# Kernel optimization log

Hardware: AMD Instinct MI355X
Metric: run time of the kernel (lower is better)

Reference implementation:

```python
import jax, jax.numpy as jnp
import numpy as np

N, D, E = 50000, 128, 800000


def setup_inputs() -> dict:
    key = jax.random.key(0)
    ks = jax.random.split(key, 12)
    x0 = jax.random.normal(ks[0], (N, D), dtype=jnp.float32)
    x1 = jax.random.normal(ks[1], (N, D), dtype=jnp.float32)
    edge_index = jax.random.randint(ks[2], (2, E), 0, N, dtype=jnp.int64)
    s = 0.05
    W1 = jax.random.normal(ks[3], (D, D), dtype=jnp.float32) * s
    b1 = jax.random.normal(ks[4], (D,), dtype=jnp.float32) * s
    W2 = jax.random.normal(ks[5], (D, D), dtype=jnp.float32) * s
    b2 = jax.random.normal(ks[6], (D,), dtype=jnp.float32) * s
    a1_w = jax.random.normal(ks[7], (D,), dtype=jnp.float32) * s
    a1_b = jax.random.normal(ks[8], (), dtype=jnp.float32) * s
    a2_w = jax.random.normal(ks[9], (D,), dtype=jnp.float32) * s
    a2_b = jax.random.normal(ks[10], (), dtype=jnp.float32) * s
    return {"x0": x0, "x1": x1, "edge_index": edge_index,
            "W1": W1, "b1": b1, "W2": W2, "b2": b2,
            "a1_w": a1_w, "a1_b": a1_b, "a2_w": a2_w, "a2_b": a2_b}


def reference(x0, x1, edge_index, W1, b1, W2, b2, a1_w, a1_b, a2_w, a2_b):
    # LeakyReLU(0.2) applied to both projections
    lrelu = lambda v: jnp.where(v >= 0, v, 0.2 * v)
    x0_i = lrelu(x0 @ W1.T + b1)          # [N, D]
    x0_j = lrelu(x0 @ W2.T + b2)          # [N, D]
    a1 = x0_i @ a1_w + a1_b               # [N]
    a2 = x0_j @ a2_w + a2_b               # [N]
    src, dst = edge_index[0], edge_index[1]
    # sigmoid(a_1 + a_2.T) evaluated only at the sparse edge indices
    att = jax.nn.sigmoid(a1[src] + a2[dst])            # [E]
    msg = att[:, None] * x0_j[dst]                     # [E, D]
    out = jax.ops.segment_sum(msg, src, num_segments=x0.shape[0])  # sparse.mm
    return out + x0
```

## Files before the change

kernel.cpp:

```cpp
#include <hip/hip_runtime.h>
#include <hip/hip_bf16.h>

typedef unsigned int u32;
typedef unsigned short u16;

#define DIM 128
#define LWS 136
#define CHUNK 2048

typedef __bf16 bfrag __attribute__((ext_vector_type(8)));
typedef float  facc  __attribute__((ext_vector_type(4)));

__device__ __forceinline__ float2 bfpair(u32 u) {
    union { u32 i; float f; } lo, hi;
    lo.i = (u & 0xFFFFu) << 16;
    hi.i = u & 0xFFFF0000u;
    return make_float2(lo.f, hi.f);
}
__device__ __forceinline__ float bf1(u16 h) {
    union { u32 i; float f; } a; a.i = ((u32)h) << 16; return a.f;
}
__device__ __forceinline__ u16 f2bf(float f) {
    __hip_bfloat16 h = __float2bfloat16(f);
    return *reinterpret_cast<u16*>(&h);
}
__device__ __forceinline__ u32 packbf(float x, float y) {
    return (u32)f2bf(x) | ((u32)f2bf(y) << 16);
}

template<bool BF16>
__device__ __forceinline__ float ldf(const void* p, int i) {
    if constexpr (BF16) return bf1(((const u16*)p)[i]);
    else                return ((const float*)p)[i];
}

template<bool BF16>
__device__ __forceinline__ bfrag ldfrag(const void* base, int row, int elt) {
    if constexpr (BF16) {
        const uint4* p = (const uint4*)((const u16*)base + (size_t)row * DIM + elt);
        return __builtin_bit_cast(bfrag, *p);
    } else {
        const float4* p = (const float4*)((const float*)base + (size_t)row * DIM + elt);
        float4 f0 = p[0], f1 = p[1];
        uint4 u = make_uint4(packbf(f0.x, f0.y), packbf(f0.z, f0.w),
                             packbf(f1.x, f1.y), packbf(f1.z, f1.w));
        return __builtin_bit_cast(bfrag, u);
    }
}

__global__ __launch_bounds__(64) void sniff_kernel(const u32* __restrict__ x0w,
                                                   const int* __restrict__ eiw,
                                                   int* __restrict__ flags) {
    int l = threadIdx.x;
    u32 w = x0w[l];
    u32 ef = (w >> 7) & 0xFF;
    bool inr = (ef >= 99 && ef <= 141);
    unsigned long long m1 = __ballot(inr);
    bool zodd = (eiw[2 * l + 1] == 0);
    unsigned long long m2 = __ballot(zodd);
    if (l == 0) {
        flags[0] = (__popcll(m1) >= 48) ? 1 : 0;
        flags[1] = (__popcll(m2) >= 32) ? 1 : 0;
    }
}

template<bool BF16>
__global__ __launch_bounds__(256) void proj_kernel(
    const void* __restrict__ x0v,
    const void* __restrict__ W1v, const void* __restrict__ b1v,
    const void* __restrict__ W2v, const void* __restrict__ b2v,
    const void* __restrict__ a1wv, const void* __restrict__ a1bv,
    const void* __restrict__ a2wv, const void* __restrict__ a2bv,
    u16* __restrict__ xj, float* __restrict__ a1, float* __restrict__ a2,
    const int* __restrict__ flags, int n, int nchunk, int bpg)
{
    if ((flags[0] != 0) != BF16) return;
    __shared__ u16 lw[128 * LWS];

    const int t   = threadIdx.x;
    const int grp = blockIdx.x / bpg;
    const int cb  = blockIdx.x % bpg;

    const void* Wv  = grp ? W2v  : W1v;
    const void* bv  = grp ? b2v  : b1v;
    const void* awv = grp ? a2wv : a1wv;
    const void* abv = grp ? a2bv : a1bv;
    float* aout     = grp ? a2   : a1;

    for (int j = t; j < 2048; j += 256) {
        int r = j >> 4, c = j & 15;
        uint4 u;
        if constexpr (BF16) {
            u = *(const uint4*)((const u16*)Wv + (size_t)r * DIM + c * 8);
        } else {
            const float4* p = (const float4*)((const float*)Wv + (size_t)r * DIM + c * 8);
            float4 f0 = p[0], f1 = p[1];
            u = make_uint4(packbf(f0.x, f0.y), packbf(f0.z, f0.w),
                           packbf(f1.x, f1.y), packbf(f1.z, f1.w));
        }
        *(uint4*)(lw + (size_t)r * LWS + c * 8) = u;
    }
    __syncthreads();

    const int wid = t >> 6, l = t & 63;
    const int chunk = cb * 4 + wid;
    if (chunk >= nchunk) return;
    const int r0 = chunk * 32;
    const int lr = l & 15;
    const int q  = l >> 4;

    bfrag a[2][4];
    #pragma unroll
    for (int rt = 0; rt < 2; ++rt) {
        int row = min(r0 + rt * 16 + lr, n - 1);
        #pragma unroll
        for (int k = 0; k < 4; ++k)
            a[rt][k] = ldfrag<BF16>(x0v, row, k * 32 + q * 8);
    }

    facc acc[2][8];
    #pragma unroll
    for (int rt = 0; rt < 2; ++rt)
        #pragma unroll
        for (int ct = 0; ct < 8; ++ct)
            acc[rt][ct] = (facc){0.f, 0.f, 0.f, 0.f};

    #pragma unroll
    for (int ct = 0; ct < 8; ++ct) {
        bfrag bb[4];
        const u16* lrow = lw + (size_t)(ct * 16 + lr) * LWS;
        #pragma unroll
        for (int k = 0; k < 4; ++k)
            bb[k] = *(const bfrag*)(lrow + k * 32 + q * 8);
        #pragma unroll
        for (int rt = 0; rt < 2; ++rt)
            #pragma unroll
            for (int k = 0; k < 4; ++k)
                acc[rt][ct] = __builtin_amdgcn_mfma_f32_16x16x32_bf16(
                    a[rt][k], bb[k], acc[rt][ct], 0, 0, 0);
    }

    float s[2][4] = {{0.f,0.f,0.f,0.f},{0.f,0.f,0.f,0.f}};
    #pragma unroll
    for (int ct = 0; ct < 8; ++ct) {
        float bc  = ldf<BF16>(bv,  ct * 16 + lr);
        float awc = ldf<BF16>(awv, ct * 16 + lr);
        #pragma unroll
        for (int rt = 0; rt < 2; ++rt)
            #pragma unroll
            for (int reg = 0; reg < 4; ++reg) {
                float v = acc[rt][ct][reg] + bc;
                v = v >= 0.f ? v : 0.2f * v;
                int row = r0 + rt * 16 + q * 4 + reg;
                if (grp && row < n)
                    xj[(size_t)row * DIM + ct * 16 + lr] = f2bf(v);
                s[rt][reg] = fmaf(v, awc, s[rt][reg]);
            }
    }
    #pragma unroll
    for (int off = 1; off < 16; off <<= 1)
        #pragma unroll
        for (int rt = 0; rt < 2; ++rt)
            #pragma unroll
            for (int reg = 0; reg < 4; ++reg)
                s[rt][reg] += __shfl_xor(s[rt][reg], off);
    if (lr == 0) {
        float ab = ldf<BF16>(abv, 0);
        #pragma unroll
        for (int rt = 0; rt < 2; ++rt)
            #pragma unroll
            for (int reg = 0; reg < 4; ++reg) {
                int row = r0 + rt * 16 + q * 4 + reg;
                if (row < n) aout[row] = s[rt][reg] + ab;
            }
    }
}


__global__ __launch_bounds__(256) void countA_kernel(
    const int* __restrict__ ei, u32* __restrict__ keys0,
    int* __restrict__ cnt, const int* __restrict__ flags, int ne, int nblk)
{
    __shared__ int h[256];
    const int b = blockIdx.x, t = threadIdx.x;
    h[t] = 0;
    __syncthreads();
    const bool i64 = flags[1] != 0;
    const int base = b * CHUNK;
    #pragma unroll
    for (int r = 0; r < CHUNK / 256; ++r) {
        int i = base + r * 256 + t;
        if (i < ne) {
            int src = i64 ? ei[2 * i] : ei[i];
            int dst = i64 ? ei[2 * (ne + i)] : ei[ne + i];
            u32 key = ((u32)src << 16) | (u32)dst;
            keys0[i] = key;
            atomicAdd(&h[(key >> 16) & 0xFF], 1);
        }
    }
    __syncthreads();
    cnt[t * nblk + b] = h[t];
}

__global__ __launch_bounds__(256) void countB_kernel(
    const u32* __restrict__ kin, int* __restrict__ cnt, int ne, int nblk)
{
    __shared__ int h[256];
    const int b = blockIdx.x, t = threadIdx.x;
    h[t] = 0;
    __syncthreads();
    const int base = b * CHUNK;
    #pragma unroll
    for (int r = 0; r < CHUNK / 256; ++r) {
        int i = base + r * 256 + t;
        if (i < ne) atomicAdd(&h[kin[i] >> 24], 1);
    }
    __syncthreads();
    cnt[t * nblk + b] = h[t];
}

__global__ __launch_bounds__(256) void scan1_kernel(
    const int* __restrict__ cnt, int* __restrict__ off,
    int* __restrict__ tot, int nblk)
{
    __shared__ int v[512];
    const int d = blockIdx.x, t = threadIdx.x;
    int c0 = (t < nblk) ? cnt[d * nblk + t] : 0;
    int c1 = (t + 256 < nblk) ? cnt[d * nblk + t + 256] : 0;
    v[t] = c0; v[t + 256] = c1;
    __syncthreads();
    for (int s = 1; s < 512; s <<= 1) {
        int a0 = v[t],      b0 = (t >= s) ? v[t - s] : 0;
        int a1 = v[t + 256], b1 = (t + 256 >= s) ? v[t + 256 - s] : 0;
        __syncthreads();
        v[t] = a0 + b0; v[t + 256] = a1 + b1;
        __syncthreads();
    }
    if (t < nblk)       off[d * nblk + t]       = v[t] - c0;
    if (t + 256 < nblk) off[d * nblk + t + 256] = v[t + 256] - c1;
    if (t == 0) tot[d] = v[511];
}

__global__ __launch_bounds__(256) void scan2_kernel(
    const int* __restrict__ tot, int* __restrict__ basev)
{
    __shared__ int v[256];
    const int t = threadIdx.x;
    int c = tot[t];
    v[t] = c;
    __syncthreads();
    for (int s = 1; s < 256; s <<= 1) {
        int a = v[t], b = (t >= s) ? v[t - s] : 0;
        __syncthreads();
        v[t] = a + b;
        __syncthreads();
    }
    basev[t] = v[t] - c;
}

__global__ __launch_bounds__(256) void reorderA_kernel(
    const u32* __restrict__ kin, u32* __restrict__ kout,
    const int* __restrict__ off, const int* __restrict__ basev,
    int ne, int nblk)
{
    __shared__ u32 kk[CHUNK];
    __shared__ int boff[256];
    __shared__ int bcnt[256];
    const int b = blockIdx.x, t = threadIdx.x;
    const int base = b * CHUNK;
    const int cntk = min(CHUNK, ne - base);
    #pragma unroll
    for (int r = 0; r < CHUNK / 256; ++r) {
        int i = r * 256 + t;
        if (i < cntk) kk[i] = kin[base + i];
    }
    boff[t] = basev[t] + off[t * nblk + b];
    bcnt[t] = 0;
    __syncthreads();
    #pragma unroll
    for (int r = 0; r < CHUNK / 256; ++r) {
        int i = r * 256 + t;
        if (i < cntk) {
            u32 key = kk[i];
            int d = (key >> 16) & 0xFF;
            int rk = atomicAdd(&bcnt[d], 1);
            kout[boff[d] + rk] = key;
        }
    }
}

__global__ __launch_bounds__(64) void reorderB_kernel(
    const u32* __restrict__ kin, u32* __restrict__ kout,
    const int* __restrict__ off, const int* __restrict__ basev,
    int ne, int nblk)
{
    __shared__ u16 M[256 * 65];
    __shared__ u32 kk[CHUNK];
    __shared__ int boff[256];
    const int b = blockIdx.x, t = threadIdx.x;
    u32* M32 = (u32*)M;
    for (int j = t; j < 256 * 65 / 2; j += 64) M32[j] = 0;
    const int base = b * CHUNK;
    const int cntk = min(CHUNK, ne - base);
    for (int r = 0; r < CHUNK / 64; ++r) {
        int i = r * 64 + t;
        if (i < cntk) kk[i] = kin[base + i];
    }
    for (int d = t; d < 256; d += 64) boff[d] = basev[d] + off[d * nblk + b];
    __syncthreads();
    const int k0 = t * (CHUNK / 64);
    for (int j = 0; j < CHUNK / 64; ++j) {
        int i = k0 + j;
        if (i < cntk) { int d = kk[i] >> 24; M[d * 65 + t] += 1; }
    }
    __syncthreads();
    for (int rr = 0; rr < 4; ++rr) {
        int d = t + rr * 64;
        int run = 0, rb = d * 65;
        for (int j = 0; j < 64; ++j) {
            int c = M[rb + j]; M[rb + j] = (u16)run; run += c;
        }
    }
    __syncthreads();
    for (int j = 0; j < CHUNK / 64; ++j) {
        int i = k0 + j;
        if (i < cntk) {
            u32 key = kk[i];
            int d = key >> 24;
            int rk = M[d * 65 + t];
            M[d * 65 + t] = (u16)(rk + 1);
            kout[boff[d] + rk] = key;
        }
    }
}

__global__ __launch_bounds__(256) void ptr_kernel(
    const u32* __restrict__ skeys, int* __restrict__ ptr, int ne, int n)
{
    int i = blockIdx.x * 256 + threadIdx.x;
    if (i >= ne) return;
    int s = (int)(skeys[i] >> 16);
    if (i == 0) {
        for (int j = 0; j <= s; ++j) ptr[j] = 0;
    } else {
        int sp = (int)(skeys[i - 1] >> 16);
        for (int j = sp + 1; j <= s; ++j) ptr[j] = i;
    }
    if (i == ne - 1) {
        for (int j = s + 1; j <= n; ++j) ptr[j] = ne;
    }
}

template<bool BF16>
__global__ __launch_bounds__(256) void gather_kernel(
    const int* __restrict__ ptr, const u32* __restrict__ skeys,
    const float* __restrict__ a1, const float* __restrict__ a2,
    const u32* __restrict__ xjw, const void* __restrict__ x0v,
    void* __restrict__ outv, const int* __restrict__ flags, int n)
{
    if ((flags[0] != 0) != BF16) return;
    int s = blockIdx.x * 4 + (threadIdx.x >> 6);
    int l = threadIdx.x & 63;
    if (s >= n) return;

    float2 acc0, acc1;
    if constexpr (BF16) acc0 = bfpair(((const u32*)x0v)[(size_t)s * 64 + l]);
    else                acc0 = ((const float2*)x0v)[(size_t)s * 64 + l];
    acc1 = make_float2(0.f, 0.f);
    const float a1s = a1[s];

    int k = ptr[s], end = ptr[s + 1];

    while (k + 8 <= end) {
        u32 r[8];
        #pragma unroll
        for (int j = 0; j < 8; ++j) r[j] = skeys[k + j];
        u32 w[8]; float av[8];
        #pragma unroll
        for (int j = 0; j < 8; ++j) w[j] = xjw[(size_t)(r[j] & 0xFFFFu) * 64 + l];
        #pragma unroll
        for (int j = 0; j < 8; ++j) av[j] = a2[r[j] & 0xFFFFu];
        #pragma unroll
        for (int j = 0; j < 8; ++j) {
            float att = 1.0f / (1.0f + __expf(-(a1s + av[j])));
            float2 xv = bfpair(w[j]);
            if (j & 1) { acc1.x = fmaf(att, xv.x, acc1.x);
                         acc1.y = fmaf(att, xv.y, acc1.y); }
            else       { acc0.x = fmaf(att, xv.x, acc0.x);
                         acc0.y = fmaf(att, xv.y, acc0.y); }
        }
        k += 8;
    }
    if (k + 4 <= end) {
        u32 r[4];
        #pragma unroll
        for (int j = 0; j < 4; ++j) r[j] = skeys[k + j];
        u32 w[4]; float av[4];
        #pragma unroll
        for (int j = 0; j < 4; ++j) w[j] = xjw[(size_t)(r[j] & 0xFFFFu) * 64 + l];
        #pragma unroll
        for (int j = 0; j < 4; ++j) av[j] = a2[r[j] & 0xFFFFu];
        #pragma unroll
        for (int j = 0; j < 4; ++j) {
            float att = 1.0f / (1.0f + __expf(-(a1s + av[j])));
            float2 xv = bfpair(w[j]);
            if (j & 1) { acc1.x = fmaf(att, xv.x, acc1.x);
                         acc1.y = fmaf(att, xv.y, acc1.y); }
            else       { acc0.x = fmaf(att, xv.x, acc0.x);
                         acc0.y = fmaf(att, xv.y, acc0.y); }
        }
        k += 4;
    }
    for (; k < end; ++k) {
        u32 cur = skeys[k];
        float att = 1.0f / (1.0f + __expf(-(a1s + a2[cur & 0xFFFFu])));
        float2 xv = bfpair(xjw[(size_t)(cur & 0xFFFFu) * 64 + l]);
        acc0.x = fmaf(att, xv.x, acc0.x);
        acc0.y = fmaf(att, xv.y, acc0.y);
    }
    acc0.x += acc1.x;
    acc0.y += acc1.y;

    if constexpr (BF16) ((u32*)outv)[(size_t)s * 64 + l] = packbf(acc0.x, acc0.y);
    else                ((float2*)outv)[(size_t)s * 64 + l] = acc0;
}

extern "C" void kernel_launch(void* const* d_in, const int* in_sizes, int n_in,
                              void* d_out, int out_size, void* d_ws, size_t ws_size,
                              hipStream_t stream)
{
    const void* x0  = d_in[0];
    const int*  ei  = (const int*)d_in[2];
    const void* W1  = d_in[3];
    const void* b1  = d_in[4];
    const void* W2  = d_in[5];
    const void* b2  = d_in[6];
    const void* a1w = d_in[7];
    const void* a1b = d_in[8];
    const void* a2w = d_in[9];
    const void* a2b = d_in[10];

    const int n = in_sizes[0] / DIM;
    const int e = in_sizes[2] / 2;
    const int nblk = (e + CHUNK - 1) / CHUNK;

    char* ws = (char*)d_ws;
    int* flags = (int*)ws;
    size_t off = 1024;
    u16* xj = (u16*)(ws + off);
    off += (size_t)n * DIM * sizeof(u16);   off = (off + 255) & ~(size_t)255;
    float* a1 = (float*)(ws + off);
    off += (size_t)n * sizeof(float);       off = (off + 255) & ~(size_t)255;
    float* a2 = (float*)(ws + off);
    off += (size_t)n * sizeof(float);       off = (off + 255) & ~(size_t)255;
    u32* keys0 = (u32*)(ws + off);
    off += (size_t)e * sizeof(u32);         off = (off + 255) & ~(size_t)255;
    u32* keys1 = (u32*)(ws + off);
    off += (size_t)e * sizeof(u32);         off = (off + 255) & ~(size_t)255;
    u32* keys2 = (u32*)(ws + off);
    off += (size_t)e * sizeof(u32);         off = (off + 255) & ~(size_t)255;
    int* cntA = (int*)(ws + off);
    off += (size_t)256 * nblk * sizeof(int); off = (off + 255) & ~(size_t)255;
    int* offA = (int*)(ws + off);
    off += (size_t)256 * nblk * sizeof(int); off = (off + 255) & ~(size_t)255;
    int* cntB = (int*)(ws + off);
    off += (size_t)256 * nblk * sizeof(int); off = (off + 255) & ~(size_t)255;
    int* offB = (int*)(ws + off);
    off += (size_t)256 * nblk * sizeof(int); off = (off + 255) & ~(size_t)255;
    int* totA = (int*)(ws + off);  off += 1024;
    int* baseA = (int*)(ws + off); off += 1024;
    int* totB = (int*)(ws + off);  off += 1024;
    int* baseB = (int*)(ws + off); off += 1024;
    int* ptr = (int*)(ws + off);
    off += (size_t)(n + 1) * sizeof(int);

    sniff_kernel<<<1, 64, 0, stream>>>((const u32*)x0, ei, flags);

    const int nchunk = (n + 31) / 32;
    const int bpg = (nchunk + 3) / 4;
    proj_kernel<true ><<<2 * bpg, 256, 0, stream>>>(x0, W1, b1, W2, b2, a1w, a1b,
                                                    a2w, a2b, xj, a1, a2, flags, n, nchunk, bpg);
    proj_kernel<false><<<2 * bpg, 256, 0, stream>>>(x0, W1, b1, W2, b2, a1w, a1b,
                                                    a2w, a2b, xj, a1, a2, flags, n, nchunk, bpg);

    countA_kernel<<<nblk, 256, 0, stream>>>(ei, keys0, cntA, flags, e, nblk);
    scan1_kernel<<<256, 256, 0, stream>>>(cntA, offA, totA, nblk);
    scan2_kernel<<<1, 256, 0, stream>>>(totA, baseA);
    reorderA_kernel<<<nblk, 256, 0, stream>>>(keys0, keys1, offA, baseA, e, nblk);
    countB_kernel<<<nblk, 256, 0, stream>>>(keys1, cntB, e, nblk);
    scan1_kernel<<<256, 256, 0, stream>>>(cntB, offB, totB, nblk);
    scan2_kernel<<<1, 256, 0, stream>>>(totB, baseB);
    reorderB_kernel<<<nblk, 64, 0, stream>>>(keys1, keys2, offB, baseB, e, nblk);
    ptr_kernel<<<(e + 255) / 256, 256, 0, stream>>>(keys2, ptr, e, n);

    int gblocks = (n + 3) / 4;
    gather_kernel<true ><<<gblocks, 256, 0, stream>>>(ptr, keys2, a1, a2,
                                                      (const u32*)xj, x0, d_out, flags, n);
    gather_kernel<false><<<gblocks, 256, 0, stream>>>(ptr, keys2, a1, a2,
                                                      (const u32*)xj, x0, d_out, flags, n);
}
```

Baseline: 230.5 us.

## Replace two-pass radix sort with one bucket pass plus per-bucket local sort

The two-pass LSD radix sort by source node (count/scan/reorder twice plus a ptr kernel) becomes a single global pass on the high byte. It is followed by one block per high-byte bucket that locally sorts by the low byte and writes the CSR row pointers directly. That bucket kernel also computes the sigmoid attention per edge and stores (dst, att) pairs, so the gather no longer reads a1/a2 or evaluates the exp. This removes several launches and a full pass over the keys, but writes 8-byte records instead of 4-byte keys, and each bucket (~3k edges) is handled by a single 256-thread block.

```diff
diff --git a/kernel.cpp b/kernel.cpp
--- a/kernel.cpp
+++ b/kernel.cpp
@@ -177,7 +177,7 @@
 }
 
 
-__global__ __launch_bounds__(256) void countA_kernel(
+__global__ __launch_bounds__(256) void countH_kernel(
     const int* __restrict__ ei, u32* __restrict__ keys0,
     int* __restrict__ cnt, const int* __restrict__ flags, int ne, int nblk)
 {
@@ -195,25 +195,8 @@
             int dst = i64 ? ei[2 * (ne + i)] : ei[ne + i];
             u32 key = ((u32)src << 16) | (u32)dst;
             keys0[i] = key;
-            atomicAdd(&h[(key >> 16) & 0xFF], 1);
+            atomicAdd(&h[key >> 24], 1);
         }
-    }
-    __syncthreads();
-    cnt[t * nblk + b] = h[t];
-}
-
-__global__ __launch_bounds__(256) void countB_kernel(
-    const u32* __restrict__ kin, int* __restrict__ cnt, int ne, int nblk)
-{
-    __shared__ int h[256];
-    const int b = blockIdx.x, t = threadIdx.x;
-    h[t] = 0;
-    __syncthreads();
-    const int base = b * CHUNK;
-    #pragma unroll
-    for (int r = 0; r < CHUNK / 256; ++r) {
-        int i = base + r * 256 + t;
-        if (i < ne) atomicAdd(&h[kin[i] >> 24], 1);
     }
     __syncthreads();
     cnt[t * nblk + b] = h[t];
@@ -258,103 +241,77 @@
     basev[t] = v[t] - c;
 }
 
-__global__ __launch_bounds__(256) void reorderA_kernel(
+__global__ __launch_bounds__(256) void reorderH_kernel(
     const u32* __restrict__ kin, u32* __restrict__ kout,
     const int* __restrict__ off, const int* __restrict__ basev,
     int ne, int nblk)
 {
-    __shared__ u32 kk[CHUNK];
     __shared__ int boff[256];
     __shared__ int bcnt[256];
     const int b = blockIdx.x, t = threadIdx.x;
     const int base = b * CHUNK;
-    const int cntk = min(CHUNK, ne - base);
-    #pragma unroll
-    for (int r = 0; r < CHUNK / 256; ++r) {
-        int i = r * 256 + t;
-        if (i < cntk) kk[i] = kin[base + i];
-    }
     boff[t] = basev[t] + off[t * nblk + b];
     bcnt[t] = 0;
     __syncthreads();
     #pragma unroll
     for (int r = 0; r < CHUNK / 256; ++r) {
-        int i = r * 256 + t;
-        if (i < cntk) {
-            u32 key = kk[i];
-            int d = (key >> 16) & 0xFF;
+        int i = base + r * 256 + t;
+        if (i < ne) {
+            u32 key = kin[i];
+            int d = key >> 24;
             int rk = atomicAdd(&bcnt[d], 1);
             kout[boff[d] + rk] = key;
         }
     }
 }
 
-__global__ __launch_bounds__(64) void reorderB_kernel(
-    const u32* __restrict__ kin, u32* __restrict__ kout,
-    const int* __restrict__ off, const int* __restrict__ basev,
-    int ne, int nblk)
-{
-    __shared__ u16 M[256 * 65];
-    __shared__ u32 kk[CHUNK];
-    __shared__ int boff[256];
+__global__ __launch_bounds__(256) void bucket_kernel(
+    const u32* __restrict__ keys1, const int* __restrict__ basev,
+    const int* __restrict__ tot, const float* __restrict__ a1,
+    const float* __restrict__ a2, int* __restrict__ ptr,
+    uint2* __restrict__ sorted, int n)
+{
+    __shared__ int cnt[256];
+    __shared__ int sc[256];
+    __shared__ int cur[256];
     const int b = blockIdx.x, t = threadIdx.x;
-    u32* M32 = (u32*)M;
-    for (int j = t; j < 256 * 65 / 2; j += 64) M32[j] = 0;
-    const int base = b * CHUNK;
-    const int cntk = min(CHUNK, ne - base);
-    for (int r = 0; r < CHUNK / 64; ++r) {
-        int i = r * 64 + t;
-        if (i < cntk) kk[i] = kin[base + i];
-    }
-    for (int d = t; d < 256; d += 64) boff[d] = basev[d] + off[d * nblk + b];
-    __syncthreads();
-    const int k0 = t * (CHUNK / 64);
-    for (int j = 0; j < CHUNK / 64; ++j) {
-        int i = k0 + j;
-        if (i < cntk) { int d = kk[i] >> 24; M[d * 65 + t] += 1; }
-    }
-    __syncthreads();
-    for (int rr = 0; rr < 4; ++rr) {
-        int d = t + rr * 64;
-        int run = 0, rb = d * 65;
-        for (int j = 0; j < 64; ++j) {
-            int c = M[rb + j]; M[rb + j] = (u16)run; run += c;
-        }
-    }
-    __syncthreads();
-    for (int j = 0; j < CHUNK / 64; ++j) {
-        int i = k0 + j;
-        if (i < cntk) {
-            u32 key = kk[i];
-            int d = key >> 24;
-            int rk = M[d * 65 + t];
-            M[d * 65 + t] = (u16)(rk + 1);
-            kout[boff[d] + rk] = key;
-        }
-    }
-}
-
-__global__ __launch_bounds__(256) void ptr_kernel(
-    const u32* __restrict__ skeys, int* __restrict__ ptr, int ne, int n)
-{
-    int i = blockIdx.x * 256 + threadIdx.x;
-    if (i >= ne) return;
-    int s = (int)(skeys[i] >> 16);
-    if (i == 0) {
-        for (int j = 0; j <= s; ++j) ptr[j] = 0;
-    } else {
-        int sp = (int)(skeys[i - 1] >> 16);
-        for (int j = sp + 1; j <= s; ++j) ptr[j] = i;
-    }
-    if (i == ne - 1) {
-        for (int j = s + 1; j <= n; ++j) ptr[j] = ne;
+    const int base = basev[b];
+    const int size = tot[b];
+    cnt[t] = 0;
+    __syncthreads();
+    for (int i = t; i < size; i += 256)
+        atomicAdd(&cnt[(keys1[base + i] >> 16) & 0xFF], 1);
+    __syncthreads();
+    int c = cnt[t];
+    sc[t] = c;
+    __syncthreads();
+    for (int s = 1; s < 256; s <<= 1) {
+        int a = sc[t], add = (t >= s) ? sc[t - s] : 0;
+        __syncthreads();
+        sc[t] = a + add;
+        __syncthreads();
+    }
+    int ex = sc[t] - c;
+    cur[t] = ex;
+    int sg = (b << 8) + t;
+    if (sg <= n) ptr[sg] = base + ex;
+    __syncthreads();
+    for (int i = t; i < size; i += 256) {
+        u32 key = keys1[base + i];
+        int j   = (key >> 16) & 0xFF;
+        int rk  = atomicAdd(&cur[j], 1);
+        int src = (int)(key >> 16);
+        int dst = (int)(key & 0xFFFFu);
+        float av  = a1[src] + a2[dst];
+        float att = 1.0f / (1.0f + __expf(-av));
+        uint2 rec; rec.x = (u32)dst; rec.y = __float_as_uint(att);
+        sorted[base + rk] = rec;
     }
 }
 
 template<bool BF16>
 __global__ __launch_bounds__(256) void gather_kernel(
-    const int* __restrict__ ptr, const u32* __restrict__ skeys,
-    const float* __restrict__ a1, const float* __restrict__ a2,
+    const int* __restrict__ ptr, const uint2* __restrict__ sorted,
     const u32* __restrict__ xjw, const void* __restrict__ x0v,
     void* __restrict__ outv, const int* __restrict__ flags, int n)
 {
@@ -367,22 +324,19 @@
     if constexpr (BF16) acc0 = bfpair(((const u32*)x0v)[(size_t)s * 64 + l]);
     else                acc0 = ((const float2*)x0v)[(size_t)s * 64 + l];
     acc1 = make_float2(0.f, 0.f);
-    const float a1s = a1[s];
 
     int k = ptr[s], end = ptr[s + 1];
 
     while (k + 8 <= end) {
-        u32 r[8];
-        #pragma unroll
-        for (int j = 0; j < 8; ++j) r[j] = skeys[k + j];
-        u32 w[8]; float av[8];
-        #pragma unroll
-        for (int j = 0; j < 8; ++j) w[j] = xjw[(size_t)(r[j] & 0xFFFFu) * 64 + l];
-        #pragma unroll
-        for (int j = 0; j < 8; ++j) av[j] = a2[r[j] & 0xFFFFu];
+        uint2 r[8];
+        #pragma unroll
+        for (int j = 0; j < 8; ++j) r[j] = sorted[k + j];
+        u32 w[8];
+        #pragma unroll
+        for (int j = 0; j < 8; ++j) w[j] = xjw[(size_t)r[j].x * 64 + l];
         #pragma unroll
         for (int j = 0; j < 8; ++j) {
-            float att = 1.0f / (1.0f + __expf(-(a1s + av[j])));
+            float att = __uint_as_float(r[j].y);
             float2 xv = bfpair(w[j]);
             if (j & 1) { acc1.x = fmaf(att, xv.x, acc1.x);
                          acc1.y = fmaf(att, xv.y, acc1.y); }
@@ -392,17 +346,15 @@
         k += 8;
     }
     if (k + 4 <= end) {
-        u32 r[4];
-        #pragma unroll
-        for (int j = 0; j < 4; ++j) r[j] = skeys[k + j];
-        u32 w[4]; float av[4];
-        #pragma unroll
-        for (int j = 0; j < 4; ++j) w[j] = xjw[(size_t)(r[j] & 0xFFFFu) * 64 + l];
-        #pragma unroll
-        for (int j = 0; j < 4; ++j) av[j] = a2[r[j] & 0xFFFFu];
+        uint2 r[4];
+        #pragma unroll
+        for (int j = 0; j < 4; ++j) r[j] = sorted[k + j];
+        u32 w[4];
+        #pragma unroll
+        for (int j = 0; j < 4; ++j) w[j] = xjw[(size_t)r[j].x * 64 + l];
         #pragma unroll
         for (int j = 0; j < 4; ++j) {
-            float att = 1.0f / (1.0f + __expf(-(a1s + av[j])));
+            float att = __uint_as_float(r[j].y);
             float2 xv = bfpair(w[j]);
             if (j & 1) { acc1.x = fmaf(att, xv.x, acc1.x);
                          acc1.y = fmaf(att, xv.y, acc1.y); }
@@ -412,9 +364,9 @@
         k += 4;
     }
     for (; k < end; ++k) {
-        u32 cur = skeys[k];
-        float att = 1.0f / (1.0f + __expf(-(a1s + a2[cur & 0xFFFFu])));
-        float2 xv = bfpair(xjw[(size_t)(cur & 0xFFFFu) * 64 + l]);
+        uint2 cur = sorted[k];
+        float att = __uint_as_float(cur.y);
+        float2 xv = bfpair(xjw[(size_t)cur.x * 64 + l]);
         acc0.x = fmaf(att, xv.x, acc0.x);
         acc0.y = fmaf(att, xv.y, acc0.y);
     }
@@ -457,22 +409,15 @@
     off += (size_t)e * sizeof(u32);         off = (off + 255) & ~(size_t)255;
     u32* keys1 = (u32*)(ws + off);
     off += (size_t)e * sizeof(u32);         off = (off + 255) & ~(size_t)255;
-    u32* keys2 = (u32*)(ws + off);
-    off += (size_t)e * sizeof(u32);         off = (off + 255) & ~(size_t)255;
-    int* cntA = (int*)(ws + off);
+    int* cntH = (int*)(ws + off);
     off += (size_t)256 * nblk * sizeof(int); off = (off + 255) & ~(size_t)255;
-    int* offA = (int*)(ws + off);
+    int* offH = (int*)(ws + off);
     off += (size_t)256 * nblk * sizeof(int); off = (off + 255) & ~(size_t)255;
-    int* cntB = (int*)(ws + off);
-    off += (size_t)256 * nblk * sizeof(int); off = (off + 255) & ~(size_t)255;
-    int* offB = (int*)(ws + off);
-    off += (size_t)256 * nblk * sizeof(int); off = (off + 255) & ~(size_t)255;
-    int* totA = (int*)(ws + off);  off += 1024;
-    int* baseA = (int*)(ws + off); off += 1024;
-    int* totB = (int*)(ws + off);  off += 1024;
-    int* baseB = (int*)(ws + off); off += 1024;
+    int* totH = (int*)(ws + off);  off += 1024;
+    int* baseH = (int*)(ws + off); off += 1024;
     int* ptr = (int*)(ws + off);
-    off += (size_t)(n + 1) * sizeof(int);
+    off += (size_t)(n + 1) * sizeof(int);   off = (off + 255) & ~(size_t)255;
+    uint2* sorted = (uint2*)(ws + off);
 
     sniff_kernel<<<1, 64, 0, stream>>>((const u32*)x0, ei, flags);
 
@@ -483,19 +428,17 @@
     proj_kernel<false><<<2 * bpg, 256, 0, stream>>>(x0, W1, b1, W2, b2, a1w, a1b,
                                                     a2w, a2b, xj, a1, a2, flags, n, nchunk, bpg);
 
-    countA_kernel<<<nblk, 256, 0, stream>>>(ei, keys0, cntA, flags, e, nblk);
-    scan1_kernel<<<256, 256, 0, stream>>>(cntA, offA, totA, nblk);
-    scan2_kernel<<<1, 256, 0, stream>>>(totA, baseA);
-    reorderA_kernel<<<nblk, 256, 0, stream>>>(keys0, keys1, offA, baseA, e, nblk);
-    countB_kernel<<<nblk, 256, 0, stream>>>(keys1, cntB, e, nblk);
-    scan1_kernel<<<256, 256, 0, stream>>>(cntB, offB, totB, nblk);
-    scan2_kernel<<<1, 256, 0, stream>>>(totB, baseB);
-    reorderB_kernel<<<nblk, 64, 0, stream>>>(keys1, keys2, offB, baseB, e, nblk);
-    ptr_kernel<<<(e + 255) / 256, 256, 0, stream>>>(keys2, ptr, e, n);
+    countH_kernel<<<nblk, 256, 0, stream>>>(ei, keys0, cntH, flags, e, nblk);
+    scan1_kernel<<<256, 256, 0, stream>>>(cntH, offH, totH, nblk);
+    scan2_kernel<<<1, 256, 0, stream>>>(totH, baseH);
+    reorderH_kernel<<<nblk, 256, 0, stream>>>(keys0, keys1, offH, baseH, e, nblk);
+    const int nbucket = (n >> 8) + 1;
+    bucket_kernel<<<nbucket, 256, 0, stream>>>(keys1, baseH, totH, a1, a2,
+                                               ptr, sorted, n);
 
     int gblocks = (n + 3) / 4;
-    gather_kernel<true ><<<gblocks, 256, 0, stream>>>(ptr, keys2, a1, a2,
-                                                      (const u32*)xj, x0, d_out, flags, n);
-    gather_kernel<false><<<gblocks, 256, 0, stream>>>(ptr, keys2, a1, a2,
-                                                      (const u32*)xj, x0, d_out, flags, n);
-}
+    gather_kernel<true ><<<gblocks, 256, 0, stream>>>(ptr, sorted, (const u32*)xj,
+                                                      x0, d_out, flags, n);
+    gather_kernel<false><<<gblocks, 256, 0, stream>>>(ptr, sorted, (const u32*)xj,
+                                                      x0, d_out, flags, n);
+}
```

Result: faster. 203.2 us (-11.8%).
